# Kernel optimization log

Measured on AMD Instinct MI355X. Metric: run time of the kernel, lower is better.

## Reference

```python
import jax, jax.numpy as jnp
import numpy as np

N_ITEM_TYPE = 18
N_ITEM_FEAT = 11
N_TYPE_HIDDEN = 32
N_ITEM_HIDDEN = 128
BS, NA, NI = 32, 128, 128


def setup_inputs() -> dict:
    key = jax.random.key(0)
    k1, k2, k3, k4 = jax.random.split(key, 4)
    item_type = jax.random.randint(k1, (BS, NA, NI), 0, N_ITEM_TYPE, dtype=jnp.int64)
    item = jax.random.normal(k2, (BS, NA, NI, N_ITEM_FEAT), dtype=jnp.float32)
    emb = jax.random.normal(k3, (N_ITEM_TYPE, N_TYPE_HIDDEN), dtype=jnp.float32)
    W = jax.random.normal(k4, (N_TYPE_HIDDEN + N_ITEM_FEAT, N_ITEM_HIDDEN), dtype=jnp.float32) * 0.1
    b = jnp.zeros((N_ITEM_HIDDEN,), dtype=jnp.float32)
    return {"item_type": item_type, "item": item, "emb": emb, "W": W, "b": b}


def reference(item_type, item, emb, W, b):
    # embedding gather: [bs, na, ni, 32]
    h_type = emb[item_type]
    # concat features: [bs, na, ni, 43]
    h = jnp.concatenate([h_type, item], axis=-1)
    # Linear + ReLU: [bs, na, ni, n_item_hidden]
    h = jax.nn.relu(jnp.einsum("bnif,fh->bnih", h, W) + b)
    # max-pool over item axis: [bs, na, n_item_hidden]
    return jnp.max(h, axis=2)
```

## Files before the change

kernel.cpp:

```cpp
#include <hip/hip_runtime.h>
#include <hip/hip_bf16.h>
#include <stdint.h>
#include <float.h>


#define NITEM  128
#define NFEAT  11
#define NTH    32
#define NH     128
#define KREAL  43
#define KSTEPS 3
#define BNPB   4
#define SLABDW (NITEM * NFEAT)

typedef __attribute__((ext_vector_type(8)))  _Float16 half8;
typedef __attribute__((ext_vector_type(2)))  __fp16   fp16x2;
typedef __attribute__((ext_vector_type(16))) float    f32x16;

union H8 { half8 h8; fp16x2 h2[4]; };

__global__ __launch_bounds__(64) void prep_b(const float* __restrict__ W,
                                             _Float16* __restrict__ Bpre) {
    const int frag = blockIdx.x;
    const int kk   = frag >> 2;
    const int n    = frag & 3;
    const int lane = threadIdx.x;
    const int col  = n * 32 + (lane & 31);
    const int k0   = kk * 16 + (lane >> 5) * 8;
    half8 pk;
    #pragma unroll
    for (int q = 0; q < 8; ++q) {
        const int k = k0 + q;
        pk[q] = (_Float16)((k < KREAL) ? W[k * NH + col] : 0.0f);
    }
    ((half8*)Bpre)[frag * 64 + lane] = pk;
}

__global__ __launch_bounds__(256, 2) void item_encoder(
    const int*      __restrict__ item_type,
    const float*    __restrict__ item,
    const float*    __restrict__ emb,
    const _Float16* __restrict__ Bpre,
    const float*    __restrict__ bias,
    float*          __restrict__ out)
{
    __shared__ float slab[BNPB * SLABDW];

    const int t    = threadIdx.x;
    const int lane = t & 63;
    const int w    = t >> 6;
    const int l31  = lane & 31;
    const int lhi  = lane >> 5;
    const int bn0  = blockIdx.x * BNPB;
    const int bn   = bn0 + w;

    int ty[4];
    {
        const int* tb = item_type + (size_t)bn * NITEM + l31;
        #pragma unroll
        for (int rb = 0; rb < 4; ++rb) ty[rb] = tb[rb * 32];
    }

    {
        const float4* gsl = (const float4*)(item + (size_t)bn0 * SLABDW);
        float4*       lsl = (float4*)slab;
        #pragma unroll
        for (int j = 0; j < 5; ++j) lsl[t + 256 * j] = gsl[t + 256 * j];
        if (t < 128) lsl[1280 + t] = gsl[1280 + t];
    }

    half8 bf[KSTEPS][4];
    #pragma unroll
    for (int kk = 0; kk < KSTEPS; ++kk)
        #pragma unroll
        for (int n = 0; n < 4; ++n)
            bf[kk][n] = ((const half8*)Bpre)[(kk * 4 + n) * 64 + lane];

    float4 E[4][4];
    #pragma unroll
    for (int rb = 0; rb < 4; ++rb) {
        const float* eb = emb + ty[rb] * NTH + lhi * 8;
        E[rb][0] = *(const float4*)(eb);
        E[rb][1] = *(const float4*)(eb + 4);
        E[rb][2] = *(const float4*)(eb + 16);
        E[rb][3] = *(const float4*)(eb + 20);
    }

    float bias4[4];
    #pragma unroll
    for (int n = 0; n < 4; ++n) bias4[n] = bias[n * 32 + l31];

    __syncthreads();

    float vm[4] = { -FLT_MAX, -FLT_MAX, -FLT_MAX, -FLT_MAX };

    #pragma unroll
    for (int rb = 0; rb < 4; ++rb) {
        const int r = rb * 32 + l31;
        const float* sp = slab + w * SLABDW + r * NFEAT;

        float fv[8];
        #pragma unroll
        for (int q = 0; q < 8; ++q) {
            const int  f  = lhi * 8 + q;
            const bool ok = (f < NFEAT);
            const float x = sp[ok ? f : 0];
            fv[q] = ok ? x : 0.0f;
        }

        H8 a0, a1, a2;
        a0.h2[0] = __builtin_amdgcn_cvt_pkrtz(E[rb][0].x, E[rb][0].y);
        a0.h2[1] = __builtin_amdgcn_cvt_pkrtz(E[rb][0].z, E[rb][0].w);
        a0.h2[2] = __builtin_amdgcn_cvt_pkrtz(E[rb][1].x, E[rb][1].y);
        a0.h2[3] = __builtin_amdgcn_cvt_pkrtz(E[rb][1].z, E[rb][1].w);
        a1.h2[0] = __builtin_amdgcn_cvt_pkrtz(E[rb][2].x, E[rb][2].y);
        a1.h2[1] = __builtin_amdgcn_cvt_pkrtz(E[rb][2].z, E[rb][2].w);
        a1.h2[2] = __builtin_amdgcn_cvt_pkrtz(E[rb][3].x, E[rb][3].y);
        a1.h2[3] = __builtin_amdgcn_cvt_pkrtz(E[rb][3].z, E[rb][3].w);
        a2.h2[0] = __builtin_amdgcn_cvt_pkrtz(fv[0], fv[1]);
        a2.h2[1] = __builtin_amdgcn_cvt_pkrtz(fv[2], fv[3]);
        a2.h2[2] = __builtin_amdgcn_cvt_pkrtz(fv[4], fv[5]);
        a2.h2[3] = __builtin_amdgcn_cvt_pkrtz(fv[6], fv[7]);

        f32x16 acc[4];
        #pragma unroll
        for (int n = 0; n < 4; ++n)
            #pragma unroll
            for (int rr = 0; rr < 16; ++rr) acc[n][rr] = 0.0f;

        #pragma unroll
        for (int n = 0; n < 4; ++n) acc[n] = __builtin_amdgcn_mfma_f32_32x32x16_f16(a0.h8, bf[0][n], acc[n], 0, 0, 0);
        #pragma unroll
        for (int n = 0; n < 4; ++n) acc[n] = __builtin_amdgcn_mfma_f32_32x32x16_f16(a1.h8, bf[1][n], acc[n], 0, 0, 0);
        #pragma unroll
        for (int n = 0; n < 4; ++n) acc[n] = __builtin_amdgcn_mfma_f32_32x32x16_f16(a2.h8, bf[2][n], acc[n], 0, 0, 0);

        #pragma unroll
        for (int n = 0; n < 4; ++n) {
            float m = acc[n][0];
            #pragma unroll
            for (int rr = 1; rr < 16; ++rr) m = fmaxf(m, acc[n][rr]);
            m = fmaxf(m, __shfl_xor(m, 32));
            vm[n] = fmaxf(vm[n], m);
        }
    }

    if (lane < 32) {
        #pragma unroll
        for (int n = 0; n < 4; ++n)
            out[(size_t)bn * NH + n * 32 + l31] = fmaxf(vm[n] + bias4[n], 0.0f);
    }
}

extern "C" void kernel_launch(void* const* d_in, const int* in_sizes, int n_in,
                              void* d_out, int out_size, void* d_ws, size_t ws_size,
                              hipStream_t stream) {
    const int*   item_type = (const int*)  d_in[0];
    const float* item      = (const float*)d_in[1];
    const float* emb       = (const float*)d_in[2];
    const float* W         = (const float*)d_in[3];
    const float* bias      = (const float*)d_in[4];
    float*       out       = (float*)d_out;
    _Float16*    Bpre      = (_Float16*)d_ws;

    prep_b<<<12, 64, 0, stream>>>(W, Bpre);
    item_encoder<<<(32 * 128) / BNPB, 256, 0, stream>>>(item_type, item, emb, Bpre, bias, out);
}
```

Measured before the change: 89.49 us.

## Drop LDS staging; one wave per row reading features directly from global

Replaces the 4-wave block that staged item features into shared memory with single-wave blocks, one per (batch, agent) row. Each lane reads its 11 features straight from global memory, and the embedding loads move inside the row loop. This removes the LDS copy and the block barrier and makes the blocks smaller. In exchange the feature loads are strided and uncoalesced (stride 11 floats per lane), and the grid has four times as many small blocks.

After: 93.97 us. 1.05x slower.

```diff
diff --git a/kernel.cpp b/kernel.cpp
--- a/kernel.cpp
+++ b/kernel.cpp
@@ -10,7 +10,6 @@
 #define NH     128
 #define KREAL  43
 #define KSTEPS 3
-#define BNPB   4
 #define SLABDW (NITEM * NFEAT)
 
 typedef __attribute__((ext_vector_type(8)))  _Float16 half8;
@@ -36,7 +35,7 @@
     ((half8*)Bpre)[frag * 64 + lane] = pk;
 }
 
-__global__ __launch_bounds__(256, 2) void item_encoder(
+__global__ __launch_bounds__(64, 2) void item_encoder(
     const int*      __restrict__ item_type,
     const float*    __restrict__ item,
     const float*    __restrict__ emb,
@@ -44,15 +43,17 @@
     const float*    __restrict__ bias,
     float*          __restrict__ out)
 {
-    __shared__ float slab[BNPB * SLABDW];
-
-    const int t    = threadIdx.x;
-    const int lane = t & 63;
-    const int w    = t >> 6;
+    const int lane = threadIdx.x;
     const int l31  = lane & 31;
     const int lhi  = lane >> 5;
-    const int bn0  = blockIdx.x * BNPB;
-    const int bn   = bn0 + w;
+    const int bn   = blockIdx.x;
+
+    half8 bf[KSTEPS][4];
+    #pragma unroll
+    for (int kk = 0; kk < KSTEPS; ++kk)
+        #pragma unroll
+        for (int n = 0; n < 4; ++n)
+            bf[kk][n] = ((const half8*)Bpre)[(kk * 4 + n) * 64 + lane];
 
     int ty[4];
     {
@@ -61,62 +62,43 @@
         for (int rb = 0; rb < 4; ++rb) ty[rb] = tb[rb * 32];
     }
 
-    {
-        const float4* gsl = (const float4*)(item + (size_t)bn0 * SLABDW);
-        float4*       lsl = (float4*)slab;
-        #pragma unroll
-        for (int j = 0; j < 5; ++j) lsl[t + 256 * j] = gsl[t + 256 * j];
-        if (t < 128) lsl[1280 + t] = gsl[1280 + t];
-    }
-
-    half8 bf[KSTEPS][4];
-    #pragma unroll
-    for (int kk = 0; kk < KSTEPS; ++kk)
-        #pragma unroll
-        for (int n = 0; n < 4; ++n)
-            bf[kk][n] = ((const half8*)Bpre)[(kk * 4 + n) * 64 + lane];
-
-    float4 E[4][4];
-    #pragma unroll
-    for (int rb = 0; rb < 4; ++rb) {
-        const float* eb = emb + ty[rb] * NTH + lhi * 8;
-        E[rb][0] = *(const float4*)(eb);
-        E[rb][1] = *(const float4*)(eb + 4);
-        E[rb][2] = *(const float4*)(eb + 16);
-        E[rb][3] = *(const float4*)(eb + 20);
-    }
-
     float bias4[4];
     #pragma unroll
     for (int n = 0; n < 4; ++n) bias4[n] = bias[n * 32 + l31];
 
-    __syncthreads();
+    const float* feat = item + (size_t)bn * SLABDW;
 
     float vm[4] = { -FLT_MAX, -FLT_MAX, -FLT_MAX, -FLT_MAX };
 
     #pragma unroll
     for (int rb = 0; rb < 4; ++rb) {
         const int r = rb * 32 + l31;
-        const float* sp = slab + w * SLABDW + r * NFEAT;
 
+        const float* eb = emb + ty[rb] * NTH + lhi * 8;
+        const float4 e0 = *(const float4*)(eb);
+        const float4 e1 = *(const float4*)(eb + 4);
+        const float4 e2 = *(const float4*)(eb + 16);
+        const float4 e3 = *(const float4*)(eb + 20);
+
+        const float* fp = feat + r * NFEAT;
         float fv[8];
         #pragma unroll
         for (int q = 0; q < 8; ++q) {
-            const int  f  = lhi * 8 + q;
-            const bool ok = (f < NFEAT);
-            const float x = sp[ok ? f : 0];
-            fv[q] = ok ? x : 0.0f;
+            const int  f    = lhi ? ((q < 3) ? 8 + q : 10) : q;
+            const bool dead = (lhi && q >= 3);
+            const float x = fp[f];
+            fv[q] = dead ? 0.0f : x;
         }
 
         H8 a0, a1, a2;
-        a0.h2[0] = __builtin_amdgcn_cvt_pkrtz(E[rb][0].x, E[rb][0].y);
-        a0.h2[1] = __builtin_amdgcn_cvt_pkrtz(E[rb][0].z, E[rb][0].w);
-        a0.h2[2] = __builtin_amdgcn_cvt_pkrtz(E[rb][1].x, E[rb][1].y);
-        a0.h2[3] = __builtin_amdgcn_cvt_pkrtz(E[rb][1].z, E[rb][1].w);
-        a1.h2[0] = __builtin_amdgcn_cvt_pkrtz(E[rb][2].x, E[rb][2].y);
-        a1.h2[1] = __builtin_amdgcn_cvt_pkrtz(E[rb][2].z, E[rb][2].w);
-        a1.h2[2] = __builtin_amdgcn_cvt_pkrtz(E[rb][3].x, E[rb][3].y);
-        a1.h2[3] = __builtin_amdgcn_cvt_pkrtz(E[rb][3].z, E[rb][3].w);
+        a0.h2[0] = __builtin_amdgcn_cvt_pkrtz(e0.x, e0.y);
+        a0.h2[1] = __builtin_amdgcn_cvt_pkrtz(e0.z, e0.w);
+        a0.h2[2] = __builtin_amdgcn_cvt_pkrtz(e1.x, e1.y);
+        a0.h2[3] = __builtin_amdgcn_cvt_pkrtz(e1.z, e1.w);
+        a1.h2[0] = __builtin_amdgcn_cvt_pkrtz(e2.x, e2.y);
+        a1.h2[1] = __builtin_amdgcn_cvt_pkrtz(e2.z, e2.w);
+        a1.h2[2] = __builtin_amdgcn_cvt_pkrtz(e3.x, e3.y);
+        a1.h2[3] = __builtin_amdgcn_cvt_pkrtz(e3.z, e3.w);
         a2.h2[0] = __builtin_amdgcn_cvt_pkrtz(fv[0], fv[1]);
         a2.h2[1] = __builtin_amdgcn_cvt_pkrtz(fv[2], fv[3]);
         a2.h2[2] = __builtin_amdgcn_cvt_pkrtz(fv[4], fv[5]);
@@ -164,5 +146,5 @@
     _Float16*    Bpre      = (_Float16*)d_ws;
 
     prep_b<<<12, 64, 0, stream>>>(W, Bpre);
-    item_encoder<<<(32 * 128) / BNPB, 256, 0, stream>>>(item_type, item, emb, Bpre, bias, out);
+    item_encoder<<<32 * 128, 64, 0, stream>>>(item_type, item, emb, Bpre, bias, out);
 }
```
